# Kernel optimization log

Hardware: AMD Instinct MI355X
Metric: run time of the kernel (lower is better)

## Reference

```python
import jax, jax.numpy as jnp
import numpy as np

N_NODES = 50000
HEADS = 4
CH = 128
NEG_SLOPE = 0.2


def _gatv2_layer(x, src, dst, Wl, Wr, att, bias):
    # x: [N, Fin]; src/dst: [E'] (self-loops already appended)
    N = x.shape[0]
    xl = (x @ Wl).reshape(N, HEADS, CH)   # source-side transform
    xr = (x @ Wr).reshape(N, HEADS, CH)   # target-side transform
    e = jax.nn.leaky_relu(xl[src] + xr[dst], NEG_SLOPE)   # [E', H, C]
    logits = jnp.einsum('ehc,hc->eh', e, att)             # [E', H]
    # segment softmax over incoming edges of each destination node
    m = jax.ops.segment_max(logits, dst, num_segments=N)
    m = jnp.where(jnp.isfinite(m), m, 0.0)
    p = jnp.exp(logits - m[dst])
    denom = jax.ops.segment_sum(p, dst, num_segments=N)
    alpha = p / denom[dst]                                # [E', H]
    out = jax.ops.segment_sum(alpha[:, :, None] * xl[src], dst, num_segments=N)
    return out.reshape(N, HEADS * CH) + bias


def setup_inputs() -> dict:
    key = jax.random.key(0)
    ks = jax.random.split(key, 12)
    E = 400000
    x = jax.random.normal(ks[0], (N_NODES, 55), dtype=jnp.float32)
    edge_index = jax.random.randint(ks[1], (2, E), 0, N_NODES, dtype=jnp.int64)
    s = 0.1
    d1, d2 = 55, HEADS * CH
    return {
        'x': x,
        'edge_index': edge_index,
        'W1l': jax.random.normal(ks[2], (d1, d2), dtype=jnp.float32) * s,
        'W1r': jax.random.normal(ks[3], (d1, d2), dtype=jnp.float32) * s,
        'att1': jax.random.normal(ks[4], (HEADS, CH), dtype=jnp.float32) * s,
        'b1': jnp.zeros((d2,), dtype=jnp.float32),
        'W2l': jax.random.normal(ks[5], (d2, d2), dtype=jnp.float32) * s,
        'W2r': jax.random.normal(ks[6], (d2, d2), dtype=jnp.float32) * s,
        'att2': jax.random.normal(ks[7], (HEADS, CH), dtype=jnp.float32) * s,
        'b2': jnp.zeros((d2,), dtype=jnp.float32),
        'Wc': jax.random.normal(ks[8], (d2, 49), dtype=jnp.float32) * s,
        'bc': jnp.zeros((49,), dtype=jnp.float32),
    }


def reference(x, edge_index, W1l, W1r, att1, b1, W2l, W2r, att2, b2, Wc, bc):
    # add self loops once (PyG GATv2Conv default add_self_loops=True)
    loops = jnp.arange(N_NODES, dtype=edge_index.dtype)
    src = jnp.concatenate([edge_index[0], loops])
    dst = jnp.concatenate([edge_index[1], loops])
    h = _gatv2_layer(x, src, dst, W1l, W1r, att1, b1)
    h = jax.nn.elu(h)  # dropout is identity in eval mode
    h = _gatv2_layer(h, src, dst, W2l, W2r, att2, b2)
    h = jax.nn.elu(h)
    # forward applies conv2 a second time (conv3 unused in source)
    h = _gatv2_layer(h, src, dst, W2l, W2r, att2, b2)
    h = jax.nn.elu(h)
    return h @ Wc + bc
```

## Files before the change

### kernel.cpp

```cpp
#include <hip/hip_runtime.h>
#include <hip/hip_bf16.h>

constexpr int NN   = 50000;
constexpr int EE   = 400000;
constexpr int EP   = 450000;
constexpr int D    = 512;
constexpr int D2   = 1024;
constexpr int F0   = 55;
constexpr int F0P  = 64;
constexpr int OUTC = 49;

typedef __hip_bfloat16 bf16;

using frag_ab  = __attribute__((ext_vector_type(8))) short;
using frag_cd16 = __attribute__((ext_vector_type(16))) float;

__device__ inline void stf(float* p, float v) { *p = v; }
__device__ inline void stf(bf16* p, float v)  { *p = __float2bfloat16(v); }

__device__ inline void unpack8(uint4 u, float* f) {
    unsigned w[4] = {u.x, u.y, u.z, u.w};
    #pragma unroll
    for (int j = 0; j < 4; ++j) {
        __hip_bfloat162 h = *(__hip_bfloat162*)&w[j];
        float2 t = __bfloat1622float2(h);
        f[2 * j] = t.x; f[2 * j + 1] = t.y;
    }
}

template <typename TC>
__global__ __launch_bounds__(256) void gemm_mfma_bt(
    const bf16* __restrict__ A,
    const bf16* __restrict__ Bt,
    TC* __restrict__ C,
    const float* __restrict__ bias,
    int M, int Ncs, int K)
{
    constexpr int BM = 128, BN = 128, BK = 32;
    __shared__ bf16 As[BM * BK];
    __shared__ bf16 Bs[BN * BK];

    int bx = blockIdx.x, by = blockIdx.y;
    if (gridDim.x == 8) {
        int bid = by * 8 + bx;
        bx = (bid >> 3) & 7;
        by = (bid & 7) + ((bid >> 6) << 3);
        if (by * BM >= M) return;
    }

    const int tid  = threadIdx.x;
    const int wave = tid >> 6;
    const int lane = tid & 63;
    const int rowBase = by * BM;
    const int colBase = bx * BN;

    frag_cd16 acc[2][2] = {};

    int arow0 = rowBase + wave * 32 + (lane >> 2);
    int arow1 = arow0 + 16;
    if (arow0 >= M) arow0 = M - 1;
    if (arow1 >= M) arow1 = M - 1;
    const bf16* gA0 = A + (size_t)arow0 * K + (lane & 3) * 8;
    const bf16* gA1 = A + (size_t)arow1 * K + (lane & 3) * 8;
    const int brow0 = colBase + wave * 32 + (lane >> 2);
    const bf16* gB0 = Bt + (size_t)brow0 * K + (lane & 3) * 8;
    const bf16* gB1 = gB0 + (size_t)16 * K;

    bf16* lA0 = &As[(wave * 32)      * BK];
    bf16* lA1 = &As[(wave * 32 + 16) * BK];
    bf16* lB0 = &Bs[(wave * 32)      * BK];
    bf16* lB1 = &Bs[(wave * 32 + 16) * BK];

    const int m32 = lane & 31;
    const int kh  = lane >> 5;
    const int wm = (wave >> 1) * 64;
    const int wn = (wave & 1) * 64;

    for (int k0 = 0; k0 < K; k0 += BK) {
        __builtin_amdgcn_global_load_lds(
            (const __attribute__((address_space(1))) void*)(gA0 + k0),
            (__attribute__((address_space(3))) void*)lA0, 16, 0, 0);
        __builtin_amdgcn_global_load_lds(
            (const __attribute__((address_space(1))) void*)(gA1 + k0),
            (__attribute__((address_space(3))) void*)lA1, 16, 0, 0);
        __builtin_amdgcn_global_load_lds(
            (const __attribute__((address_space(1))) void*)(gB0 + k0),
            (__attribute__((address_space(3))) void*)lB0, 16, 0, 0);
        __builtin_amdgcn_global_load_lds(
            (const __attribute__((address_space(1))) void*)(gB1 + k0),
            (__attribute__((address_space(3))) void*)lB1, 16, 0, 0);
        __syncthreads();

        #pragma unroll
        for (int kk = 0; kk < 2; ++kk) {
            const int koff = kk * 16 + kh * 8;
            frag_ab a[2], b[2];
            #pragma unroll
            for (int i = 0; i < 2; ++i)
                a[i] = *(const frag_ab*)&As[(wm + i * 32 + m32) * BK + koff];
            #pragma unroll
            for (int j = 0; j < 2; ++j)
                b[j] = *(const frag_ab*)&Bs[(wn + j * 32 + m32) * BK + koff];
            #pragma unroll
            for (int i = 0; i < 2; ++i)
                #pragma unroll
                for (int j = 0; j < 2; ++j)
                    acc[i][j] = __builtin_amdgcn_mfma_f32_32x32x16_bf16(
                        a[i], b[j], acc[i][j], 0, 0, 0);
        }
        __syncthreads();
    }

    #pragma unroll
    for (int i = 0; i < 2; ++i) {
        #pragma unroll
        for (int r = 0; r < 16; ++r) {
            int row = rowBase + wm + i * 32 + (r & 3) + 8 * (r >> 2) + 4 * kh;
            if (row >= M) continue;
            #pragma unroll
            for (int j = 0; j < 2; ++j) {
                int col = colBase + wn + j * 32 + m32;
                if (col >= Ncs) continue;
                float v = acc[i][j][r];
                if (bias) v += bias[col];
                stf(&C[(size_t)row * Ncs + col], v);
            }
        }
    }
}

__global__ void convert_transpose2(const float* __restrict__ W0,
                                   const float* __restrict__ W1,
                                   bf16* __restrict__ Wt) {
    __shared__ float tile[32][33];
    const float* W = blockIdx.z ? W1 : W0;
    bf16* dst = Wt + (size_t)blockIdx.z * D * D;
    int bn = blockIdx.x * 32, bk = blockIdx.y * 32;
    int tx = threadIdx.x & 31, ty = threadIdx.x >> 5;
    #pragma unroll
    for (int i = 0; i < 32; i += 8)
        tile[ty + i][tx] = W[(size_t)(bk + ty + i) * D + bn + tx];
    __syncthreads();
    #pragma unroll
    for (int i = 0; i < 32; i += 8)
        dst[(size_t)(bn + ty + i) * D + bk + tx] = __float2bfloat16(tile[tx][ty + i]);
}

__global__ void pad_convert_x(const float* __restrict__ x, bf16* __restrict__ Xp) {
    int idx = blockIdx.x * blockDim.x + threadIdx.x;
    if (idx >= NN * F0P) return;
    int n = idx >> 6, t = idx & 63;
    float v = (t < F0) ? x[n * F0 + t] : 0.f;
    Xp[idx] = __float2bfloat16(v);
}

__global__ void conv_transpose_w1(const float* __restrict__ Wl,
                                  const float* __restrict__ Wr,
                                  bf16* __restrict__ Wt) {
    const float* W = blockIdx.y ? Wr : Wl;
    bf16* dst = Wt + (size_t)blockIdx.y * D * F0P;
    int n = blockIdx.x;
    int k = threadIdx.x;
    float v = (k < F0) ? W[(size_t)k * D + n] : 0.f;
    dst[n * F0P + k] = __float2bfloat16(v);
}

__global__ void conv_transpose_wc(const float* __restrict__ W, bf16* __restrict__ Wt) {
    int n = blockIdx.x;
    for (int k = threadIdx.x; k < D; k += blockDim.x) {
        float v = (n < OUTC) ? W[(size_t)k * OUTC + n] : 0.f;
        Wt[(size_t)n * D + k] = __float2bfloat16(v);
    }
}

__global__ void zero_ints(int* __restrict__ p, int n) {
    int i = blockIdx.x * blockDim.x + threadIdx.x;
    if (i < n) p[i] = 0;
}

__global__ void count_dst(const int* __restrict__ dstIdx, int* __restrict__ cnt) {
    int e = blockIdx.x * blockDim.x + threadIdx.x;
    if (e >= EP) return;
    int dst = (e < EE) ? dstIdx[e] : (e - EE);
    atomicAdd(&cnt[dst], 1);
}

__global__ void scan_blocks(const int* __restrict__ cnt, int* __restrict__ off,
                            int* __restrict__ bsum) {
    __shared__ int sh[1024];
    int i = blockIdx.x * 1024 + threadIdx.x;
    int v = (i < NN) ? cnt[i] : 0;
    sh[threadIdx.x] = v;
    __syncthreads();
    #pragma unroll
    for (int d = 1; d < 1024; d <<= 1) {
        int t = (threadIdx.x >= d) ? sh[threadIdx.x - d] : 0;
        __syncthreads();
        sh[threadIdx.x] += t;
        __syncthreads();
    }
    if (i < NN) off[i] = sh[threadIdx.x] - v;
    if (threadIdx.x == 1023) bsum[blockIdx.x] = sh[1023];
}

__global__ void scan_bsums(int* __restrict__ bsum, int* __restrict__ bbase,
                           int* __restrict__ off, int nb) {
    int lane = threadIdx.x;
    int orig = (lane < nb) ? bsum[lane] : 0;
    int v = orig;
    #pragma unroll
    for (int d = 1; d < 64; d <<= 1) {
        int t = __shfl_up(v, d);
        if (lane >= d) v += t;
    }
    if (lane < nb) bbase[lane] = v - orig;
    if (lane == 63) off[NN] = v;
}

__global__ void add_base(int* __restrict__ off, const int* __restrict__ bbase) {
    int i = blockIdx.x * 1024 + threadIdx.x;
    if (blockIdx.x == 0 || i >= NN) return;
    off[i] += bbase[blockIdx.x];
}

__global__ void fill_srcpos(const int* __restrict__ srcIdx, const int* __restrict__ dstIdx,
                            const int* __restrict__ off, int* __restrict__ cnt,
                            int* __restrict__ srcPos) {
    int e = blockIdx.x * blockDim.x + threadIdx.x;
    if (e >= EP) return;
    int dst = (e < EE) ? dstIdx[e] : (e - EE);
    int src = (e < EE) ? srcIdx[e] : (e - EE);
    int pos = off[dst] + atomicAdd(&cnt[dst], 1);
    srcPos[pos] = src;
}

__global__ __launch_bounds__(256) void gat_edge_fused(
    const bf16* __restrict__ XLR, const float* __restrict__ att,
    const int* __restrict__ off, const int* __restrict__ srcPos,
    const float* __restrict__ bias, bf16* __restrict__ Hout)
{
    int v = blockIdx.x * 4 + (threadIdx.x >> 6);
    if (v >= NN) return;
    int lane = threadIdx.x & 63;

    uint4 ru = *(const uint4*)(XLR + (size_t)v * D2 + D + lane * 8);
    float xr[8]; unpack8(ru, xr);
    const float4* a4 = (const float4*)(att + lane * 8);
    float4 aa = a4[0], ab = a4[1];
    float at[8] = {aa.x, aa.y, aa.z, aa.w, ab.x, ab.y, ab.z, ab.w};

    int s0 = off[v], s1 = off[v + 1];
    float den = 0.f;
    float acc[8] = {};

    uint4 lb0 = {0, 0, 0, 0}, lb1 = {0, 0, 0, 0};
    if (s0 < s1)     lb0 = *(const uint4*)(XLR + (size_t)srcPos[s0] * D2 + lane * 8);
    if (s0 + 1 < s1) lb1 = *(const uint4*)(XLR + (size_t)srcPos[s0 + 1] * D2 + lane * 8);

    for (int i = s0; i < s1; ++i) {
        uint4 cur = lb0;
        lb0 = lb1;
        if (i + 2 < s1)
            lb1 = *(const uint4*)(XLR + (size_t)srcPos[i + 2] * D2 + lane * 8);

        float xl[8]; unpack8(cur, xl);
        float sa = 0.f, sb = 0.f;
        #pragma unroll
        for (int j = 0; j < 4; ++j) {
            float t = xl[j] + xr[j];
            t = fmaxf(t, 0.2f * t);
            sa = fmaf(t, at[j], sa);
        }
        #pragma unroll
        for (int j = 4; j < 8; ++j) {
            float t = xl[j] + xr[j];
            t = fmaxf(t, 0.2f * t);
            sb = fmaf(t, at[j], sb);
        }
        float s = sa + sb;
        s += __shfl_xor(s, 1);
        s += __shfl_xor(s, 2);
        s += __shfl_xor(s, 4);
        s += __shfl_xor(s, 8);
        s = fminf(fmaxf(s, -60.f), 60.f);
        float p = __expf(s);
        den += p;
        #pragma unroll
        for (int j = 0; j < 8; ++j) acc[j] = fmaf(p, xl[j], acc[j]);
    }
    float r = 1.f / den;

    const float4* b4 = (const float4*)(bias + lane * 8);
    float4 ba = b4[0], bb = b4[1];
    float bi[8] = {ba.x, ba.y, ba.z, ba.w, bb.x, bb.y, bb.z, bb.w};
    uint4 ou;
    unsigned* ow = (unsigned*)&ou;
    #pragma unroll
    for (int j = 0; j < 4; ++j) {
        float o0 = acc[2 * j] * r + bi[2 * j];
        float o1 = acc[2 * j + 1] * r + bi[2 * j + 1];
        o0 = o0 > 0.f ? o0 : (__expf(o0) - 1.f);
        o1 = o1 > 0.f ? o1 : (__expf(o1) - 1.f);
        __hip_bfloat162 h{__float2bfloat16(o0), __float2bfloat16(o1)};
        ow[j] = *(unsigned*)&h;
    }
    *(uint4*)(Hout + (size_t)v * D + lane * 8) = ou;
}

extern "C" void kernel_launch(void* const* d_in, const int* in_sizes, int n_in,
                              void* d_out, int out_size, void* d_ws, size_t ws_size,
                              hipStream_t stream) {
    const float* x    = (const float*)d_in[0];
    const int*   ei   = (const int*)d_in[1];
    const float* W1l  = (const float*)d_in[2];
    const float* W1r  = (const float*)d_in[3];
    const float* att1 = (const float*)d_in[4];
    const float* b1   = (const float*)d_in[5];
    const float* W2l  = (const float*)d_in[6];
    const float* W2r  = (const float*)d_in[7];
    const float* att2 = (const float*)d_in[8];
    const float* b2   = (const float*)d_in[9];
    const float* Wc   = (const float*)d_in[10];
    const float* bc   = (const float*)d_in[11];
    float* out = (float*)d_out;

    const int* srcIdx = ei;
    const int* dstIdx = ei + EE;

    constexpr int NB = (NN + 1023) / 1024;

    bf16* XLR  = (bf16*)d_ws;
    bf16* Hb   = XLR + (size_t)NN * D2;
    bf16* Xpad = Hb + (size_t)NN * D;
    bf16* W2T  = Xpad + (size_t)NN * F0P;
    bf16* W1T  = W2T + (size_t)D2 * D;
    bf16* WcT  = W1T + (size_t)D2 * F0P;
    int* cnt   = (int*)(WcT + (size_t)128 * D);
    int* cnt2  = cnt + NN;
    int* off   = cnt2 + NN;
    int* srcPos= off + (NN + 1);
    int* bsum  = srcPos + EP;
    int* bbase = bsum + NB;

    zero_ints<<<(2 * NN + 255) / 256, 256, 0, stream>>>(cnt, 2 * NN);
    count_dst<<<(EP + 255) / 256, 256, 0, stream>>>(dstIdx, cnt);
    scan_blocks<<<NB, 1024, 0, stream>>>(cnt, off, bsum);
    scan_bsums<<<1, 64, 0, stream>>>(bsum, bbase, off, NB);
    add_base<<<NB, 1024, 0, stream>>>(off, bbase);
    fill_srcpos<<<(EP + 255) / 256, 256, 0, stream>>>(srcIdx, dstIdx, off, cnt2, srcPos);

    dim3 ctGrid(D / 32, D / 32, 2);
    convert_transpose2<<<ctGrid, 256, 0, stream>>>(W2l, W2r, W2T);
    dim3 w1Grid(D, 2);
    conv_transpose_w1<<<w1Grid, F0P, 0, stream>>>(W1l, W1r, W1T);
    conv_transpose_wc<<<128, 256, 0, stream>>>(Wc, WcT);
    pad_convert_x<<<(NN * F0P + 255) / 256, 256, 0, stream>>>(x, Xpad);

    dim3 gemmGrid(D2 / 128, ((NN + 127) / 128 + 7) / 8 * 8 + 8);
    int nodeBlocks = (NN + 3) / 4;

    gemm_mfma_bt<bf16><<<gemmGrid, 256, 0, stream>>>(Xpad, W1T, XLR, nullptr, NN, D2, F0P);
    gat_edge_fused<<<nodeBlocks, 256, 0, stream>>>(XLR, att1, off, srcPos, b1, Hb);

    for (int rep = 0; rep < 2; ++rep) {
        gemm_mfma_bt<bf16><<<gemmGrid, 256, 0, stream>>>(Hb, W2T, XLR, nullptr, NN, D2, D);
        gat_edge_fused<<<nodeBlocks, 256, 0, stream>>>(XLR, att2, off, srcPos, b2, Hb);
    }

    dim3 gridc(1, (NN + 127) / 128);
    gemm_mfma_bt<float><<<gridc, 256, 0, stream>>>(Hb, WcT, out, bc, NN, OUTC, D);
}
```

Before: 612.8 us.

## Triple-buffer LDS tiles in MFMA GEMM with async global-to-LDS prefetch

Converts the GEMM main loop from a single LDS buffer with two barriers per K step to a three-slot ring buffer. Loads for tile t+2 are issued before computing tile t, with vmcnt waits and one barrier per iteration. The aim is to hide global load latency behind MFMA work. In exchange it triples LDS use, which may lower occupancy, and it assumes K/BK >= 2.

New measurement: 618.5 us. About the same (+0.9%).

```diff
diff --git a/kernel.cpp b/kernel.cpp
--- a/kernel.cpp
+++ b/kernel.cpp
@@ -37,8 +37,8 @@
     int M, int Ncs, int K)
 {
     constexpr int BM = 128, BN = 128, BK = 32;
-    __shared__ bf16 As[BM * BK];
-    __shared__ bf16 Bs[BN * BK];
+    __shared__ __align__(16) bf16 As[3][BM * BK];
+    __shared__ __align__(16) bf16 Bs[3][BN * BK];
 
     int bx = blockIdx.x, by = blockIdx.y;
     if (gridDim.x == 8) {
@@ -66,41 +66,44 @@
     const bf16* gB0 = Bt + (size_t)brow0 * K + (lane & 3) * 8;
     const bf16* gB1 = gB0 + (size_t)16 * K;
 
-    bf16* lA0 = &As[(wave * 32)      * BK];
-    bf16* lA1 = &As[(wave * 32 + 16) * BK];
-    bf16* lB0 = &Bs[(wave * 32)      * BK];
-    bf16* lB1 = &Bs[(wave * 32 + 16) * BK];
+    const int aoff0 = (wave * 32)      * BK;
+    const int aoff1 = (wave * 32 + 16) * BK;
 
     const int m32 = lane & 31;
     const int kh  = lane >> 5;
     const int wm = (wave >> 1) * 64;
     const int wn = (wave & 1) * 64;
 
-    for (int k0 = 0; k0 < K; k0 += BK) {
+    auto stage = [&](int t) {
+        const int slot = t % 3;
+        const int kc = t * BK;
         __builtin_amdgcn_global_load_lds(
-            (const __attribute__((address_space(1))) void*)(gA0 + k0),
-            (__attribute__((address_space(3))) void*)lA0, 16, 0, 0);
+            (const __attribute__((address_space(1))) void*)(gA0 + kc),
+            (__attribute__((address_space(3))) void*)(As[slot] + aoff0), 16, 0, 0);
         __builtin_amdgcn_global_load_lds(
-            (const __attribute__((address_space(1))) void*)(gA1 + k0),
-            (__attribute__((address_space(3))) void*)lA1, 16, 0, 0);
+            (const __attribute__((address_space(1))) void*)(gA1 + kc),
+            (__attribute__((address_space(3))) void*)(As[slot] + aoff1), 16, 0, 0);
         __builtin_amdgcn_global_load_lds(
-            (const __attribute__((address_space(1))) void*)(gB0 + k0),
-            (__attribute__((address_space(3))) void*)lB0, 16, 0, 0);
+            (const __attribute__((address_space(1))) void*)(gB0 + kc),
+            (__attribute__((address_space(3))) void*)(Bs[slot] + aoff0), 16, 0, 0);
         __builtin_amdgcn_global_load_lds(
-            (const __attribute__((address_space(1))) void*)(gB1 + k0),
-            (__attribute__((address_space(3))) void*)lB1, 16, 0, 0);
-        __syncthreads();
-
+            (const __attribute__((address_space(1))) void*)(gB1 + kc),
+            (__attribute__((address_space(3))) void*)(Bs[slot] + aoff1), 16, 0, 0);
+    };
+
+    auto compute = [&](int slot) {
+        const bf16* Ab = As[slot];
+        const bf16* Bb = Bs[slot];
         #pragma unroll
         for (int kk = 0; kk < 2; ++kk) {
             const int koff = kk * 16 + kh * 8;
             frag_ab a[2], b[2];
             #pragma unroll
             for (int i = 0; i < 2; ++i)
-                a[i] = *(const frag_ab*)&As[(wm + i * 32 + m32) * BK + koff];
+                a[i] = *(const frag_ab*)&Ab[(wm + i * 32 + m32) * BK + koff];
             #pragma unroll
             for (int j = 0; j < 2; ++j)
-                b[j] = *(const frag_ab*)&Bs[(wn + j * 32 + m32) * BK + koff];
+                b[j] = *(const frag_ab*)&Bb[(wn + j * 32 + m32) * BK + koff];
             #pragma unroll
             for (int i = 0; i < 2; ++i)
                 #pragma unroll
@@ -108,8 +111,28 @@
                     acc[i][j] = __builtin_amdgcn_mfma_f32_32x32x16_bf16(
                         a[i], b[j], acc[i][j], 0, 0, 0);
         }
-        __syncthreads();
-    }
+    };
+
+    const int nt = K / BK;
+    stage(0);
+    stage(1);
+
+    for (int t = 0; t < nt - 2; ++t) {
+        asm volatile("s_waitcnt vmcnt(4)" ::: "memory");
+        __builtin_amdgcn_s_barrier();
+        asm volatile("" ::: "memory");
+        stage(t + 2);
+        asm volatile("" ::: "memory");
+        compute(t % 3);
+    }
+    asm volatile("s_waitcnt vmcnt(4)" ::: "memory");
+    __builtin_amdgcn_s_barrier();
+    asm volatile("" ::: "memory");
+    compute((nt - 2) % 3);
+    asm volatile("s_waitcnt vmcnt(0)" ::: "memory");
+    __builtin_amdgcn_s_barrier();
+    asm volatile("" ::: "memory");
+    compute((nt - 1) % 3);
 
     #pragma unroll
     for (int i = 0; i < 2; ++i) {
```

## Rewrite GEMM as 256x128 tile, 8-wave, triple-buffered pipelined MFMA kernel

Applied to the files above, without the earlier changes.

Replaces the single-buffered 128x128 GEMM with a 512-thread kernel using 256x128 tiles, BK=64 and a three-slot LDS ring. Global-to-LDS loads for stage s+2 are issued while the current stage computes, and the LDS layout is XOR-swizzled to avoid bank conflicts. The kernel switches to 16x16x32 MFMA and uses setprio around the compute phases. The aim is to hide memory latency and raise MFMA utilisation in the node-feature GEMMs. The cost is more LDS (about 144KB), which limits occupancy, and K is now a compile-time template parameter. The classifier GEMM wastes most of its N tile for 49 columns, and B rows beyond Ncs may be read out of bounds if WcT is not padded.

Result: no change. 606.3 us (-1.1%).

```diff
diff --git a/kernel.cpp b/kernel.cpp
--- a/kernel.cpp
+++ b/kernel.cpp
@@ -13,7 +13,7 @@
 typedef __hip_bfloat16 bf16;
 
 using frag_ab  = __attribute__((ext_vector_type(8))) short;
-using frag_cd16 = __attribute__((ext_vector_type(16))) float;
+using frag_cd4 = __attribute__((ext_vector_type(4))) float;
 
 __device__ inline void stf(float* p, float v) { *p = v; }
 __device__ inline void stf(bf16* p, float v)  { *p = __float2bfloat16(v); }
@@ -28,100 +28,161 @@
     }
 }
 
-template <typename TC>
-__global__ __launch_bounds__(256) void gemm_mfma_bt(
+template <typename TC, int NS>
+__global__ __launch_bounds__(512) void gemm_8p(
     const bf16* __restrict__ A,
     const bf16* __restrict__ Bt,
     TC* __restrict__ C,
     const float* __restrict__ bias,
-    int M, int Ncs, int K)
+    int M, int Ncs)
 {
-    constexpr int BM = 128, BN = 128, BK = 32;
-    __shared__ bf16 As[BM * BK];
-    __shared__ bf16 Bs[BN * BK];
+    constexpr int K  = NS * 64;
+    constexpr int BM = 256, BN = 128, BK = 64;
+    __shared__ __align__(16) bf16 As[3][BM * BK];
+    __shared__ __align__(16) bf16 Bs[3][BN * BK];
 
     int bx = blockIdx.x, by = blockIdx.y;
     if (gridDim.x == 8) {
         int bid = by * 8 + bx;
         bx = (bid >> 3) & 7;
         by = (bid & 7) + ((bid >> 6) << 3);
-        if (by * BM >= M) return;
-    }
-
-    const int tid  = threadIdx.x;
-    const int wave = tid >> 6;
-    const int lane = tid & 63;
+    }
+    if (by * BM >= M) return;
+
+    const int tid = threadIdx.x;
+    const int w   = tid >> 6;
+    const int l   = tid & 63;
     const int rowBase = by * BM;
     const int colBase = bx * BN;
 
-    frag_cd16 acc[2][2] = {};
-
-    int arow0 = rowBase + wave * 32 + (lane >> 2);
-    int arow1 = arow0 + 16;
-    if (arow0 >= M) arow0 = M - 1;
-    if (arow1 >= M) arow1 = M - 1;
-    const bf16* gA0 = A + (size_t)arow0 * K + (lane & 3) * 8;
-    const bf16* gA1 = A + (size_t)arow1 * K + (lane & 3) * 8;
-    const int brow0 = colBase + wave * 32 + (lane >> 2);
-    const bf16* gB0 = Bt + (size_t)brow0 * K + (lane & 3) * 8;
-    const bf16* gB1 = gB0 + (size_t)16 * K;
-
-    bf16* lA0 = &As[(wave * 32)      * BK];
-    bf16* lA1 = &As[(wave * 32 + 16) * BK];
-    bf16* lB0 = &Bs[(wave * 32)      * BK];
-    bf16* lB1 = &Bs[(wave * 32 + 16) * BK];
-
-    const int m32 = lane & 31;
-    const int kh  = lane >> 5;
-    const int wm = (wave >> 1) * 64;
-    const int wn = (wave & 1) * 64;
-
-    for (int k0 = 0; k0 < K; k0 += BK) {
-        __builtin_amdgcn_global_load_lds(
-            (const __attribute__((address_space(1))) void*)(gA0 + k0),
-            (__attribute__((address_space(3))) void*)lA0, 16, 0, 0);
-        __builtin_amdgcn_global_load_lds(
-            (const __attribute__((address_space(1))) void*)(gA1 + k0),
-            (__attribute__((address_space(3))) void*)lA1, 16, 0, 0);
-        __builtin_amdgcn_global_load_lds(
-            (const __attribute__((address_space(1))) void*)(gB0 + k0),
-            (__attribute__((address_space(3))) void*)lB0, 16, 0, 0);
-        __builtin_amdgcn_global_load_lds(
-            (const __attribute__((address_space(1))) void*)(gB1 + k0),
-            (__attribute__((address_space(3))) void*)lB1, 16, 0, 0);
-        __syncthreads();
-
-        #pragma unroll
-        for (int kk = 0; kk < 2; ++kk) {
-            const int koff = kk * 16 + kh * 8;
-            frag_ab a[2], b[2];
-            #pragma unroll
-            for (int i = 0; i < 2; ++i)
-                a[i] = *(const frag_ab*)&As[(wm + i * 32 + m32) * BK + koff];
-            #pragma unroll
-            for (int j = 0; j < 2; ++j)
-                b[j] = *(const frag_ab*)&Bs[(wn + j * 32 + m32) * BK + koff];
-            #pragma unroll
-            for (int i = 0; i < 2; ++i)
+    const bf16* gA[4];
+    #pragma unroll
+    for (int j = 0; j < 4; ++j) {
+        int c = j * 512 + tid;
+        int row = c >> 3, chs = (c & 7) ^ (row & 7);
+        int ar = rowBase + row; if (ar >= M) ar = M - 1;
+        gA[j] = A + (size_t)ar * K + chs * 8;
+    }
+    const bf16* gB[2];
+    #pragma unroll
+    for (int j = 0; j < 2; ++j) {
+        int c = j * 512 + tid;
+        int row = c >> 3, chs = (c & 7) ^ (row & 7);
+        gB[j] = Bt + (size_t)(colBase + row) * K + chs * 8;
+    }
+
+    const int l15 = l & 15, l4 = l >> 4;
+    const int wm = (w >> 1) * 64;
+    const int wn = (w & 1) * 64;
+    int aoff[4][2], boff[4][2];
+    #pragma unroll
+    for (int i = 0; i < 4; ++i) {
+        int ra = wm + i * 16 + l15;
+        int rb = wn + i * 16 + l15;
+        #pragma unroll
+        for (int ks = 0; ks < 2; ++ks) {
+            aoff[i][ks] = ra * BK + (((ks * 4 + l4) ^ (ra & 7)) * 8);
+            boff[i][ks] = rb * BK + (((ks * 4 + l4) ^ (rb & 7)) * 8);
+        }
+    }
+
+    frag_cd4 acc[4][4] = {};
+
+    auto stage = [&](int s, int p) {
+        int slot = s % 3;
+        if (p < 4) {
+            bf16* dst = &As[slot][(p * 512 + w * 64) * 8];
+            __builtin_amdgcn_global_load_lds(
+                (const __attribute__((address_space(1))) void*)(gA[p] + s * BK),
+                (__attribute__((address_space(3))) void*)dst, 16, 0, 0);
+        } else {
+            int j = p - 4;
+            bf16* dst = &Bs[slot][(j * 512 + w * 64) * 8];
+            __builtin_amdgcn_global_load_lds(
+                (const __attribute__((address_space(1))) void*)(gB[j] + s * BK),
+                (__attribute__((address_space(3))) void*)dst, 16, 0, 0);
+        }
+    };
+
+    #pragma unroll
+    for (int p = 0; p < 6; ++p) stage(0, p);
+    if (NS > 1) {
+        #pragma unroll
+        for (int p = 0; p < 6; ++p) stage(1, p);
+    }
+
+    #pragma unroll
+    for (int s = 0; s < NS; ++s) {
+        if (s + 1 < NS) asm volatile("s_waitcnt vmcnt(6)" ::: "memory");
+        else            asm volatile("s_waitcnt vmcnt(0)" ::: "memory");
+        __builtin_amdgcn_s_barrier();
+        asm volatile("" ::: "memory");
+
+        const bf16* Ab = As[s % 3];
+        const bf16* Bb = Bs[s % 3];
+
+        frag_ab bfr[4][2];
+        #pragma unroll
+        for (int ni = 0; ni < 4; ++ni)
+            #pragma unroll
+            for (int ks = 0; ks < 2; ++ks)
+                bfr[ni][ks] = *(const frag_ab*)&Bb[boff[ni][ks]];
+        frag_ab afr[2][2];
+        #pragma unroll
+        for (int mi = 0; mi < 2; ++mi)
+            #pragma unroll
+            for (int ks = 0; ks < 2; ++ks)
+                afr[mi][ks] = *(const frag_ab*)&Ab[aoff[mi][ks]];
+        if (s + 2 < NS) { stage(s + 2, 0); stage(s + 2, 1); stage(s + 2, 2); }
+
+        __builtin_amdgcn_s_barrier();
+        asm volatile("" ::: "memory");
+        __builtin_amdgcn_s_setprio(1);
+        #pragma unroll
+        for (int mi = 0; mi < 2; ++mi)
+            #pragma unroll
+            for (int ni = 0; ni < 4; ++ni)
                 #pragma unroll
-                for (int j = 0; j < 2; ++j)
-                    acc[i][j] = __builtin_amdgcn_mfma_f32_32x32x16_bf16(
-                        a[i], b[j], acc[i][j], 0, 0, 0);
-        }
-        __syncthreads();
-    }
-
-    #pragma unroll
-    for (int i = 0; i < 2; ++i) {
-        #pragma unroll
-        for (int r = 0; r < 16; ++r) {
-            int row = rowBase + wm + i * 32 + (r & 3) + 8 * (r >> 2) + 4 * kh;
+                for (int ks = 0; ks < 2; ++ks)
+                    acc[mi][ni] = __builtin_amdgcn_mfma_f32_16x16x32_bf16(
+                        afr[mi][ks], bfr[ni][ks], acc[mi][ni], 0, 0, 0);
+        __builtin_amdgcn_s_setprio(0);
+        __builtin_amdgcn_s_barrier();
+        asm volatile("" ::: "memory");
+
+        frag_ab afr2[2][2];
+        #pragma unroll
+        for (int mi = 0; mi < 2; ++mi)
+            #pragma unroll
+            for (int ks = 0; ks < 2; ++ks)
+                afr2[mi][ks] = *(const frag_ab*)&Ab[aoff[mi + 2][ks]];
+        if (s + 2 < NS) { stage(s + 2, 3); stage(s + 2, 4); stage(s + 2, 5); }
+
+        __builtin_amdgcn_s_barrier();
+        asm volatile("" ::: "memory");
+        __builtin_amdgcn_s_setprio(1);
+        #pragma unroll
+        for (int mi = 0; mi < 2; ++mi)
+            #pragma unroll
+            for (int ni = 0; ni < 4; ++ni)
+                #pragma unroll
+                for (int ks = 0; ks < 2; ++ks)
+                    acc[mi + 2][ni] = __builtin_amdgcn_mfma_f32_16x16x32_bf16(
+                        afr2[mi][ks], bfr[ni][ks], acc[mi + 2][ni], 0, 0, 0);
+        __builtin_amdgcn_s_setprio(0);
+    }
+
+    #pragma unroll
+    for (int mi = 0; mi < 4; ++mi) {
+        #pragma unroll
+        for (int r = 0; r < 4; ++r) {
+            int row = rowBase + wm + mi * 16 + l4 * 4 + r;
             if (row >= M) continue;
             #pragma unroll
-            for (int j = 0; j < 2; ++j) {
-                int col = colBase + wn + j * 32 + m32;
+            for (int ni = 0; ni < 4; ++ni) {
+                int col = colBase + wn + ni * 16 + l15;
                 if (col >= Ncs) continue;
-                float v = acc[i][j][r];
+                float v = acc[mi][ni][r];
                 if (bias) v += bias[col];
                 stf(&C[(size_t)row * Ncs + col], v);
             }
@@ -356,17 +417,18 @@
     conv_transpose_wc<<<128, 256, 0, stream>>>(Wc, WcT);
     pad_convert_x<<<(NN * F0P + 255) / 256, 256, 0, stream>>>(x, Xpad);
 
-    dim3 gemmGrid(D2 / 128, ((NN + 127) / 128 + 7) / 8 * 8 + 8);
+    int gy = (((NN + 255) / 256) + 7) / 8 * 8 + 8;
+    dim3 gemmGrid(D2 / 128, gy);
     int nodeBlocks = (NN + 3) / 4;
 
-    gemm_mfma_bt<bf16><<<gemmGrid, 256, 0, stream>>>(Xpad, W1T, XLR, nullptr, NN, D2, F0P);
+    gemm_8p<bf16, 1><<<gemmGrid, 512, 0, stream>>>(Xpad, W1T, XLR, nullptr, NN, D2);
     gat_edge_fused<<<nodeBlocks, 256, 0, stream>>>(XLR, att1, off, srcPos, b1, Hb);
 
     for (int rep = 0; rep < 2; ++rep) {
-        gemm_mfma_bt<bf16><<<gemmGrid, 256, 0, stream>>>(Hb, W2T, XLR, nullptr, NN, D2, D);
+        gemm_8p<bf16, 8><<<gemmGrid, 512, 0, stream>>>(Hb, W2T, XLR, nullptr, NN, D2);
         gat_edge_fused<<<nodeBlocks, 256, 0, stream>>>(XLR, att2, off, srcPos, b2, Hb);
     }
 
-    dim3 gridc(1, (NN + 127) / 128);
-    gemm_mfma_bt<float><<<gridc, 256, 0, stream>>>(Hb, WcT, out, bc, NN, OUTC, D);
-}
+    dim3 gridc(1, (NN + 255) / 256);
+    gemm_8p<float, 8><<<gridc, 512, 0, stream>>>(Hb, WcT, out, bc, NN, OUTC);
+}
```
